# Optimization experiments

Measured on AMD Instinct MI355X. Metric: run time of the kernel, lower is better.

The kernel has to match this reference:

```python
import jax, jax.numpy as jnp
import numpy as np

B, L, D = 4, 1024, 768
H, Dh = 12, 64
W_ONE_SIDED = 512


def setup_inputs() -> dict:
    key = jax.random.key(0)
    ks = jax.random.split(key, 14)
    std = 0.02
    def lin(k):
        return jax.random.normal(k, (D, D), jnp.float32) * std
    inp = {
        "hidden_states": jax.random.normal(ks[0], (B, L, D), jnp.float32),
        "Wq": lin(ks[1]), "bq": jnp.zeros((D,), jnp.float32),
        "Wk": lin(ks[2]), "bk": jnp.zeros((D,), jnp.float32),
        "Wv": lin(ks[3]), "bv": jnp.zeros((D,), jnp.float32),
        "Wqg": lin(ks[4]), "bqg": jnp.zeros((D,), jnp.float32),
        "Wkg": lin(ks[5]), "bkg": jnp.zeros((D,), jnp.float32),
        "Wvg": lin(ks[6]), "bvg": jnp.zeros((D,), jnp.float32),
    }
    pos = jnp.arange(L)
    # last 64 positions padded; first 8 tokens are global (CLS-like)
    inp["is_index_masked"] = jnp.broadcast_to(pos >= L - 64, (B, L))
    inp["is_index_global_attn"] = jnp.broadcast_to(pos < 8, (B, L))
    return inp


def _split_heads(x):
    # [B, L, D] -> [B, L, H, Dh]
    return x.reshape(B, L, H, Dh)


def reference(hidden_states, Wq, bq, Wk, bk, Wv, bv, Wqg, bqg, Wkg, bkg, Wvg, bvg,
              is_index_masked, is_index_global_attn):
    scale = 1.0 / np.sqrt(Dh)
    x = hidden_states
    Ql = _split_heads(x @ Wq + bq)
    Kl = _split_heads(x @ Wk + bk)
    Vl = _split_heads(x @ Wv + bv)
    Qg = _split_heads(x @ Wqg + bqg)
    Kg = _split_heads(x @ Wkg + bkg)
    Vg = _split_heads(x @ Wvg + bvg)

    neg_inf = jnp.finfo(x.dtype).min
    not_masked = ~is_index_masked
    not_global = ~is_index_global_attn

    # ---- local branch: doubled-K scores [B,H,L,2L] (first half: global-key
    # columns, second half: banded local-key columns), joint softmax ----
    s = jnp.einsum('bqhd,bkhd->bhqk', Ql, Kl) * scale  # [B,H,L,L]
    idx = jnp.arange(L)
    band = jnp.abs(idx[None, :] - idx[:, None]) <= W_ONE_SIDED  # [L,L]
    global_valid = (is_index_global_attn & not_masked)[:, None, None, :]      # [B,1,1,L]
    local_valid = (band[None, :, :] & (not_masked & not_global)[:, None, :])[:, None, :, :]  # [B,1,L,L]
    s_first = jnp.where(global_valid, s, neg_inf)
    s_second = jnp.where(local_valid, s, neg_inf)
    scores_local = jnp.concatenate([s_first, s_second], axis=-1)  # [B,H,L,2L]
    probs = jax.nn.softmax(scores_local.astype(jnp.float32), axis=-1).astype(x.dtype)
    probs = jnp.where(is_index_masked[:, None, :, None], 0.0, probs)
    # (p1 + p2) @ V  ==  p1 @ V + p2 @ V  since K/V are duplicated
    p_sum = probs[..., :L] + probs[..., L:]
    attn_local = jnp.einsum('bhqk,bkhd->bqhd', p_sum, Vl).reshape(B, L, D)

    # ---- global branch: full attention over global projections ----
    sg = jnp.einsum('bqhd,bkhd->bhqk', Qg, Kg) * scale
    sg = jnp.where(is_index_masked[:, None, None, :], neg_inf, sg)
    pg = jax.nn.softmax(sg.astype(jnp.float32), axis=-1).astype(x.dtype)
    pg = jnp.where(is_index_masked[:, None, :, None], 0.0, pg)
    attn_global = jnp.einsum('bhqk,bkhd->bqhd', pg, Vg).reshape(B, L, D)

    # ---- gated combine: global tokens take the global-attention output ----
    output = jnp.where(is_index_global_attn[:, :, None], attn_global, attn_local)
    return output
```

## Files before the change

### kernel.cpp

```cpp
#include <hip/hip_runtime.h>
#include <stdint.h>
#include <math.h>

#define LSEQ 1024
#define NB 4
#define DM 768
#define NHEAD 12
#define HD 64
#define LVALID 960
#define WIN 512

typedef unsigned short u16;
typedef __attribute__((ext_vector_type(8))) short s16x8;
typedef __attribute__((ext_vector_type(4))) float f32x4;

__device__ __forceinline__ u16 f2bf(float f) {
  union { float f; uint32_t u; } v; v.f = f;
  uint32_t r = v.u + 0x7fffu + ((v.u >> 16) & 1u);
  return (u16)(r >> 16);
}
__device__ __forceinline__ float bf2f(u16 h) {
  union { uint32_t u; float f; } v; v.u = ((uint32_t)h) << 16;
  return v.f;
}
__device__ __forceinline__ int swz8(int row, int chunk) {
  return row * 8 + (chunk ^ (row & 7));
}

__device__ __forceinline__ void gload_lds16(const void* g, void* l) {
  __builtin_amdgcn_global_load_lds(
      (const __attribute__((address_space(1))) unsigned int*)g,
      (__attribute__((address_space(3))) unsigned int*)l, 16, 0, 0);
}

struct WPtrs { const float* w[6]; };
struct GemmPtrs { const u16* wt[6]; const float* bias[6]; u16* out[6]; };

__global__ __launch_bounds__(256) void prep(const float* __restrict__ x, u16* __restrict__ xb,
                                            WPtrs P, u16* __restrict__ wtb) {
  int bi = blockIdx.x;
  if (bi >= 864) {
    int i = ((bi - 864) * 256 + threadIdx.x) * 8;
    float4 a = *(const float4*)(x + i);
    float4 bq = *(const float4*)(x + i + 4);
    u16 t[8];
    t[0] = f2bf(a.x); t[1] = f2bf(a.y); t[2] = f2bf(a.z); t[3] = f2bf(a.w);
    t[4] = f2bf(bq.x); t[5] = f2bf(bq.y); t[6] = f2bf(bq.z); t[7] = f2bf(bq.w);
    *(uint4*)(xb + i) = *(uint4*)t;
    return;
  }
  int mat = bi / 144, rem = bi - mat * 144;
  int gx = rem % 12, gy = rem / 12;
  const float* W = P.w[mat];
  u16* Wt = wtb + (size_t)mat * DM * DM;
  __shared__ u16 tile[64][72];
  int k0 = gx * 64, n0 = gy * 64;
  int r4 = threadIdx.x >> 4;
  int c4 = (threadIdx.x & 15) * 4;
#pragma unroll
  for (int it = 0; it < 4; it++) {
    int r = it * 16 + r4;
    float4 v = *(const float4*)(W + (size_t)(k0 + r) * DM + n0 + c4);
    tile[c4 + 0][r] = f2bf(v.x);
    tile[c4 + 1][r] = f2bf(v.y);
    tile[c4 + 2][r] = f2bf(v.z);
    tile[c4 + 3][r] = f2bf(v.w);
  }
  __syncthreads();
  int rw = threadIdx.x >> 3, cw = (threadIdx.x & 7) * 8;
#pragma unroll
  for (int it = 0; it < 2; it++) {
    int r = it * 32 + rw;
    *(uint4*)(Wt + (size_t)(n0 + r) * DM + k0 + cw) = *(uint4*)&tile[r][cw];
  }
}

__global__ __launch_bounds__(256) void gemm6(const u16* __restrict__ Xb, GemmPtrs P,
                                             u16* __restrict__ Vt) {
  int mat = blockIdx.z;
  int m0 = blockIdx.x * 128, n0 = blockIdx.y * 128;
  if (mat == 3 && (m0 & 1023) != 0) return;
  __shared__ u16 SMEM[128 * 64 * 2];
  u16* As = SMEM;
  u16* Bs = SMEM + 128 * 64;
  const u16* Wt = P.wt[mat];
  int tid = threadIdx.x;
  int w = tid >> 6, lane = tid & 63, qd = lane >> 4, l16 = lane & 15;
  int wm = w & 1, wn = w >> 1;
  f32x4 acc[4][4];
  const f32x4 fz = {0.f, 0.f, 0.f, 0.f};
#pragma unroll
  for (int i = 0; i < 4; i++)
#pragma unroll
    for (int j = 0; j < 4; j++) acc[i][j] = fz;

  int rowS[4], colS[4];
#pragma unroll
  for (int i = 0; i < 4; i++) {
    int s = (w * 4 + i) * 64 + lane;
    rowS[i] = s >> 3;
    colS[i] = ((s & 7) ^ (rowS[i] & 7)) * 8;
  }

  for (int kt = 0; kt < DM; kt += 64) {
    __syncthreads();
#pragma unroll
    for (int i = 0; i < 4; i++)
      gload_lds16(Xb + (size_t)(m0 + rowS[i]) * DM + kt + colS[i],
                  As + (size_t)(w * 4 + i) * 64 * 8);
#pragma unroll
    for (int i = 0; i < 4; i++)
      gload_lds16(Wt + (size_t)(n0 + rowS[i]) * DM + kt + colS[i],
                  Bs + (size_t)(w * 4 + i) * 64 * 8);
    __syncthreads();
#pragma unroll
    for (int ks = 0; ks < 2; ks++) {
      s16x8 af[4], bf[4];
#pragma unroll
      for (int mi = 0; mi < 4; mi++)
        af[mi] = *(const s16x8*)(As + swz8(wm * 64 + mi * 16 + l16, ks * 4 + qd) * 8);
#pragma unroll
      for (int ni = 0; ni < 4; ni++)
        bf[ni] = *(const s16x8*)(Bs + swz8(wn * 64 + ni * 16 + l16, ks * 4 + qd) * 8);
#pragma unroll
      for (int mi = 0; mi < 4; mi++)
#pragma unroll
        for (int ni = 0; ni < 4; ni++)
          acc[mi][ni] = __builtin_amdgcn_mfma_f32_16x16x32_bf16(af[mi], bf[ni], acc[mi][ni], 0, 0, 0);
    }
  }

  const float* bias = P.bias[mat];
  u16* outp = P.out[mat];
  int bb = m0 >> 10, t0 = m0 & 1023;
  __syncthreads();
  u16* Cs = SMEM;
#pragma unroll
  for (int ni = 0; ni < 4; ni++) {
    int n = wn * 64 + ni * 16 + l16;
    float bvl = bias[n0 + n];
#pragma unroll
    for (int mi = 0; mi < 4; mi++) {
      int mb = wm * 64 + mi * 16 + qd * 4;
      u16 pk[4];
#pragma unroll
      for (int r = 0; r < 4; r++) {
        u16 v = f2bf(acc[mi][ni][r] + bvl);
        Cs[(mb + r) * 128 + n] = v;
        pk[r] = v;
      }
      if (mat == 2) {
        int gn = n0 + n, hh = gn >> 6, dd = gn & 63;
        *(uint2*)(Vt + ((size_t)(bb * NHEAD + hh) * HD + dd) * LSEQ + t0 + mb) =
            *(uint2*)pk;
      }
    }
  }
  __syncthreads();
#pragma unroll
  for (int it = 0; it < 8; it++) {
    int c = it * 256 + tid;
    int row = c >> 4, col = c & 15;
    *(uint4*)(outp + (size_t)(m0 + row) * DM + n0 + col * 8) = ((const uint4*)Cs)[c];
  }
}

__global__ __launch_bounds__(128) void attn_local(
    const u16* __restrict__ Qb, const u16* __restrict__ Kb,
    const u16* __restrict__ Vt, float* __restrict__ out) {
  int q0 = blockIdx.x * 32, h = blockIdx.y, b = blockIdx.z;
  __shared__ u16 Ks[64 * 64], Vs[64 * 64];
  __shared__ u16 Ps[2][16 * 64];
  int tid = threadIdx.x, w = tid >> 6, lane = tid & 63, qd = lane >> 4, l16 = lane & 15;

  int rowK[4], colK[4];
#pragma unroll
  for (int i = 0; i < 4; i++) {
    int s = (w * 4 + i) * 64 + lane;
    rowK[i] = s >> 3;
    colK[i] = ((s & 7) ^ (rowK[i] & 7)) * 8;
  }

  const u16* qrow = Qb + (size_t)(b * LSEQ + q0 + w * 16 + l16) * DM + h * HD;
  s16x8 af0 = *(const s16x8*)(qrow + qd * 8);
  s16x8 af1 = *(const s16x8*)(qrow + 32 + qd * 8);

  float l_part[4] = {0.f, 0.f, 0.f, 0.f};
  f32x4 aO[4];
  const f32x4 fz = {0.f, 0.f, 0.f, 0.f};
#pragma unroll
  for (int nt = 0; nt < 4; nt++) aO[nt] = fz;

  for (int c = 0; c < 16; c++) {
    int kb = c * 64;
    if (c > 0 && !(kb < LVALID && kb + 63 >= q0 - WIN && kb <= q0 + 31 + WIN)) continue;
    __syncthreads();
#pragma unroll
    for (int i = 0; i < 4; i++) {
      gload_lds16(Kb + (size_t)(b * LSEQ + kb + rowK[i]) * DM + h * HD + colK[i],
                  Ks + (size_t)(w * 4 + i) * 512);
      gload_lds16(Vt + (size_t)((b * NHEAD + h) * HD + rowK[i]) * LSEQ + kb + colK[i],
                  Vs + (size_t)(w * 4 + i) * 512);
    }
    __syncthreads();

    float p[4][4];
#pragma unroll
    for (int nt = 0; nt < 4; nt++) {
      s16x8 bk0 = *(const s16x8*)(Ks + swz8(nt * 16 + l16, qd) * 8);
      s16x8 bk1 = *(const s16x8*)(Ks + swz8(nt * 16 + l16, 4 + qd) * 8);
      f32x4 s = fz;
      s = __builtin_amdgcn_mfma_f32_16x16x32_bf16(af0, bk0, s, 0, 0, 0);
      s = __builtin_amdgcn_mfma_f32_16x16x32_bf16(af1, bk1, s, 0, 0, 0);
      int k = kb + nt * 16 + l16;
#pragma unroll
      for (int r = 0; r < 4; r++) {
        int q = q0 + w * 16 + qd * 4 + r;
        bool valid = (k < 8) || (k < LVALID && (k - q) <= WIN && (q - k) <= WIN);
        float sv = valid ? s[r] * 0.125f : -1e30f;
        p[nt][r] = __expf(sv);
        l_part[r] += p[nt][r];
      }
    }

#pragma unroll
    for (int nt = 0; nt < 4; nt++) {
      int chunk = nt * 2 + (l16 >> 3);
      int within = l16 & 7;
#pragma unroll
      for (int r = 0; r < 4; r++) {
        int qrow2 = qd * 4 + r;
        Ps[w][swz8(qrow2, chunk) * 8 + within] = f2bf(p[nt][r]);
      }
    }

    s16x8 pf0 = *(const s16x8*)(&Ps[w][0] + swz8(l16, qd) * 8);
    s16x8 pf1 = *(const s16x8*)(&Ps[w][0] + swz8(l16, 4 + qd) * 8);
#pragma unroll
    for (int nt = 0; nt < 4; nt++) {
      s16x8 v0 = *(const s16x8*)(Vs + swz8(nt * 16 + l16, qd) * 8);
      s16x8 v1 = *(const s16x8*)(Vs + swz8(nt * 16 + l16, 4 + qd) * 8);
      aO[nt] = __builtin_amdgcn_mfma_f32_16x16x32_bf16(pf0, v0, aO[nt], 0, 0, 0);
      aO[nt] = __builtin_amdgcn_mfma_f32_16x16x32_bf16(pf1, v1, aO[nt], 0, 0, 0);
    }
  }

#pragma unroll
  for (int off = 1; off < 16; off <<= 1)
#pragma unroll
    for (int r = 0; r < 4; r++) l_part[r] += __shfl_xor(l_part[r], off);
  float inv[4];
#pragma unroll
  for (int r = 0; r < 4; r++) inv[r] = 1.0f / l_part[r];
#pragma unroll
  for (int nt = 0; nt < 4; nt++)
#pragma unroll
    for (int r = 0; r < 4; r++) {
      int q = q0 + w * 16 + qd * 4 + r;
      out[(size_t)(b * LSEQ + q) * DM + h * HD + nt * 16 + l16] = aO[nt][r] * inv[r];
    }
}

__global__ __launch_bounds__(256) void attn_global(
    const u16* __restrict__ Qgb, const u16* __restrict__ Kgb,
    const u16* __restrict__ Vgb, float* __restrict__ out) {
  int h = blockIdx.x, b = blockIdx.y;
  __shared__ float p_lds[8][960];
  __shared__ float partial[4][8][64];
  int tid = threadIdx.x, w = tid >> 6, lane = tid & 63, qd = lane >> 4, l16 = lane & 15;

  {
    float4 z = {0.f, 0.f, 0.f, 0.f};
#pragma unroll
    for (int it = 0; it < 4; it++) {
      int idx = it * 256 + tid;
      int r = idx >> 4, cc = idx & 15;
      *(float4*)(out + (size_t)(b * LSEQ + LVALID + r) * DM + h * HD + cc * 4) = z;
    }
  }

  const u16* qbase = Qgb + (size_t)(b * LSEQ + l16) * DM + h * HD;
  s16x8 af0 = *(const s16x8*)(qbase + qd * 8);
  s16x8 af1 = *(const s16x8*)(qbase + 32 + qd * 8);
  const f32x4 fz = {0.f, 0.f, 0.f, 0.f};
#pragma unroll
  for (int t = 0; t < 15; t++) {
    int kb = (w + 4 * t) * 16;
    const u16* kbase = Kgb + (size_t)(b * LSEQ + kb + l16) * DM + h * HD;
    s16x8 bk0 = *(const s16x8*)(kbase + qd * 8);
    s16x8 bk1 = *(const s16x8*)(kbase + 32 + qd * 8);
    f32x4 s = fz;
    s = __builtin_amdgcn_mfma_f32_16x16x32_bf16(af0, bk0, s, 0, 0, 0);
    s = __builtin_amdgcn_mfma_f32_16x16x32_bf16(af1, bk1, s, 0, 0, 0);
    if (qd < 2) {
#pragma unroll
      for (int r = 0; r < 4; r++)
        p_lds[qd * 4 + r][kb + l16] = s[r] * 0.125f;
    }
  }
  __syncthreads();

#pragma unroll
  for (int qi = 0; qi < 2; qi++) {
    int q = w * 2 + qi;
    float m = -1e30f;
#pragma unroll
    for (int ki = 0; ki < 15; ki++) m = fmaxf(m, p_lds[q][ki * 64 + lane]);
#pragma unroll
    for (int off = 1; off < 64; off <<= 1) m = fmaxf(m, __shfl_xor(m, off));
    float e[15], ssum = 0.f;
#pragma unroll
    for (int ki = 0; ki < 15; ki++) {
      e[ki] = __expf(p_lds[q][ki * 64 + lane] - m);
      ssum += e[ki];
    }
#pragma unroll
    for (int off = 1; off < 64; off <<= 1) ssum += __shfl_xor(ssum, off);
    float inv = 1.0f / ssum;
#pragma unroll
    for (int ki = 0; ki < 15; ki++) p_lds[q][ki * 64 + lane] = e[ki] * inv;
  }
  __syncthreads();

  float acc[8] = {0.f, 0.f, 0.f, 0.f, 0.f, 0.f, 0.f, 0.f};
  const u16* vcol = Vgb + (size_t)b * LSEQ * DM + h * HD + lane;
  for (int kg = 0; kg < 60; kg++) {
    int k0 = w * 240 + kg * 4;
    float v0 = bf2f(vcol[(size_t)(k0 + 0) * DM]);
    float v1 = bf2f(vcol[(size_t)(k0 + 1) * DM]);
    float v2 = bf2f(vcol[(size_t)(k0 + 2) * DM]);
    float v3 = bf2f(vcol[(size_t)(k0 + 3) * DM]);
#pragma unroll
    for (int q = 0; q < 8; q++) {
      float4 p4 = *(const float4*)&p_lds[q][k0];
      acc[q] += p4.x * v0 + p4.y * v1 + p4.z * v2 + p4.w * v3;
    }
  }
#pragma unroll
  for (int q = 0; q < 8; q++) partial[w][q][lane] = acc[q];
  __syncthreads();
#pragma unroll
  for (int i = 0; i < 2; i++) {
    int idx = tid + 256 * i;
    int q = idx >> 6, d = idx & 63;
    float sum = partial[0][q][d] + partial[1][q][d] + partial[2][q][d] + partial[3][q][d];
    out[(size_t)(b * LSEQ + q) * DM + h * HD + d] = sum;
  }
}

extern "C" void kernel_launch(void* const* d_in, const int* in_sizes, int n_in,
                              void* d_out, int out_size, void* d_ws, size_t ws_size,
                              hipStream_t stream) {
  const float* x = (const float*)d_in[0];
  float* out = (float*)d_out;
  char* ws = (char*)d_ws;

  const size_t XB_SZ = (size_t)4096 * DM * 2;
  const size_t WT_SZ = (size_t)6 * DM * DM * 2;
  const size_t MAT_SZ = (size_t)4096 * DM;
  u16* Xb = (u16*)ws;
  u16* Wt = (u16*)(ws + XB_SZ);
  u16* QKV = (u16*)(ws + XB_SZ + WT_SZ);
  u16* Vt = (u16*)(ws + XB_SZ + WT_SZ + (size_t)6 * MAT_SZ * 2);

  u16* Ql = QKV + 0 * MAT_SZ;
  u16* Kl = QKV + 1 * MAT_SZ;
  u16* Vl = QKV + 2 * MAT_SZ;
  u16* Qg = QKV + 3 * MAT_SZ;
  u16* Kg = QKV + 4 * MAT_SZ;
  u16* Vg = QKV + 5 * MAT_SZ;

  WPtrs wp;
  wp.w[0] = (const float*)d_in[1];
  wp.w[1] = (const float*)d_in[3];
  wp.w[2] = (const float*)d_in[5];
  wp.w[3] = (const float*)d_in[7];
  wp.w[4] = (const float*)d_in[9];
  wp.w[5] = (const float*)d_in[11];
  prep<<<2400, 256, 0, stream>>>(x, Xb, wp, Wt);

  GemmPtrs gp;
  const int bidx[6] = {2, 4, 6, 8, 10, 12};
  u16* outs[6] = {Ql, Kl, Vl, Qg, Kg, Vg};
  for (int i = 0; i < 6; i++) {
    gp.wt[i] = Wt + (size_t)i * DM * DM;
    gp.bias[i] = (const float*)d_in[bidx[i]];
    gp.out[i] = outs[i];
  }
  gemm6<<<dim3(32, 6, 6), 256, 0, stream>>>(Xb, gp, Vt);

  attn_local<<<dim3(30, 12, 4), 128, 0, stream>>>(Ql, Kl, Vt, out);
  attn_global<<<dim3(12, 4), 256, 0, stream>>>(Qg, Kg, Vg, out);
}
```

Baseline: 193.3 us.

## Restructure projection GEMM into 256x256 tiles with double-buffered async LDS prefetch

Rewrites the six-way projection GEMM to use 256x256 output tiles with 512 threads per block. A double-buffered LDS pipeline issues direct global-to-LDS loads for the next k-tile while MFMAs run on the current one. The work is split into four sub-phases with explicit barriers, waitcnt and setprio to interleave loads and matrix math. This cuts the block count to roughly one wave on the device and raises operand reuse per LDS load. In exchange it needs 128KB of LDS per block, limiting occupancy to one block per CU, and depends on fragile hand-placed waits.

```diff
diff --git a/kernel.cpp b/kernel.cpp
--- a/kernel.cpp
+++ b/kernel.cpp
@@ -32,6 +32,16 @@
       (const __attribute__((address_space(1))) unsigned int*)g,
       (__attribute__((address_space(3))) unsigned int*)l, 16, 0, 0);
 }
+
+#define BARW()                                  \
+  do {                                          \
+    asm volatile("" ::: "memory");              \
+    __builtin_amdgcn_s_barrier();               \
+    asm volatile("" ::: "memory");              \
+  } while (0)
+#define LGKM0() asm volatile("s_waitcnt lgkmcnt(0)" ::: "memory")
+#define VMC4() asm volatile("s_waitcnt vmcnt(4)" ::: "memory")
+#define VMC0() asm volatile("s_waitcnt vmcnt(0)" ::: "memory")
 
 struct WPtrs { const float* w[6]; };
 struct GemmPtrs { const u16* wt[6]; const float* bias[6]; u16* out[6]; };
@@ -75,78 +85,165 @@
   }
 }
 
-__global__ __launch_bounds__(256) void gemm6(const u16* __restrict__ Xb, GemmPtrs P,
-                                             u16* __restrict__ Vt) {
+__global__ __launch_bounds__(512, 2) void gemm6(const u16* __restrict__ Xb, GemmPtrs P,
+                                                u16* __restrict__ Vt) {
   int mat = blockIdx.z;
-  int m0 = blockIdx.x * 128, n0 = blockIdx.y * 128;
+  int m0 = blockIdx.x * 256, n0 = blockIdx.y * 256;
   if (mat == 3 && (m0 & 1023) != 0) return;
-  __shared__ u16 SMEM[128 * 64 * 2];
-  u16* As = SMEM;
-  u16* Bs = SMEM + 128 * 64;
+  __shared__ __align__(16) u16 SMEM[65536];
   const u16* Wt = P.wt[mat];
   int tid = threadIdx.x;
   int w = tid >> 6, lane = tid & 63, qd = lane >> 4, l16 = lane & 15;
-  int wm = w & 1, wn = w >> 1;
-  f32x4 acc[4][4];
+  int wm = w >> 2, wn = w & 3;
+  int cx = l16 & 7;
+
+  f32x4 acc[8][4];
   const f32x4 fz = {0.f, 0.f, 0.f, 0.f};
 #pragma unroll
-  for (int i = 0; i < 4; i++)
+  for (int i = 0; i < 8; i++)
 #pragma unroll
     for (int j = 0; j < 4; j++) acc[i][j] = fz;
 
-  int rowS[4], colS[4];
-#pragma unroll
-  for (int i = 0; i < 4; i++) {
-    int s = (w * 4 + i) * 64 + lane;
-    rowS[i] = s >> 3;
-    colS[i] = ((s & 7) ^ (rowS[i] & 7)) * 8;
-  }
-
-  for (int kt = 0; kt < DM; kt += 64) {
-    __syncthreads();
-#pragma unroll
-    for (int i = 0; i < 4; i++)
-      gload_lds16(Xb + (size_t)(m0 + rowS[i]) * DM + kt + colS[i],
-                  As + (size_t)(w * 4 + i) * 64 * 8);
-#pragma unroll
-    for (int i = 0; i < 4; i++)
-      gload_lds16(Wt + (size_t)(n0 + rowS[i]) * DM + kt + colS[i],
-                  Bs + (size_t)(w * 4 + i) * 64 * 8);
-    __syncthreads();
-#pragma unroll
-    for (int ks = 0; ks < 2; ks++) {
-      s16x8 af[4], bf[4];
-#pragma unroll
-      for (int mi = 0; mi < 4; mi++)
-        af[mi] = *(const s16x8*)(As + swz8(wm * 64 + mi * 16 + l16, ks * 4 + qd) * 8);
-#pragma unroll
-      for (int ni = 0; ni < 4; ni++)
-        bf[ni] = *(const s16x8*)(Bs + swz8(wn * 64 + ni * 16 + l16, ks * 4 + qd) * 8);
-#pragma unroll
-      for (int mi = 0; mi < 4; mi++)
-#pragma unroll
-        for (int ni = 0; ni < 4; ni++)
-          acc[mi][ni] = __builtin_amdgcn_mfma_f32_16x16x32_bf16(af[mi], bf[ni], acc[mi][ni], 0, 0, 0);
-    }
-  }
+  int aoff[2][2], boff[2][2];
+#pragma unroll
+  for (int j = 0; j < 2; j++) {
+    int s = j * 512 + tid;
+    int row = s >> 3;
+    int col = ((s & 7) ^ (row & 7)) * 8;
+#pragma unroll
+    for (int h = 0; h < 2; h++) {
+      aoff[j][h] = (m0 + h * 128 + row) * DM + col;
+      boff[j][h] = (n0 + h * 128 + row) * DM + col;
+    }
+  }
+
+  auto stageA = [&](int t, int h) {
+#pragma unroll
+    for (int j = 0; j < 2; j++)
+      gload_lds16(Xb + (size_t)aoff[j][h] + t * 64,
+                  &SMEM[(t & 1) * 32768 + h * 8192 + (j * 512 + w * 64) * 8]);
+  };
+  auto stageB = [&](int t, int h) {
+#pragma unroll
+    for (int j = 0; j < 2; j++)
+      gload_lds16(Wt + (size_t)boff[j][h] + t * 64,
+                  &SMEM[(t & 1) * 32768 + 16384 + h * 8192 + (j * 512 + w * 64) * 8]);
+  };
+
+  stageA(0, 0); stageA(0, 1);
+  stageB(0, 0); stageB(0, 1);
+  stageB(1, 0); stageB(1, 1);
+  VMC4();
+  BARW();
+
+  const int rB = (wn & 1) * 64 + l16;
+
+  auto tile = [&](int u) {
+    const int buf = u & 1;
+    const u16* Ab = &SMEM[buf * 32768 + wm * 8192];
+    const u16* Bb = &SMEM[buf * 32768 + 16384 + (wn >> 1) * 8192];
+    s16x8 af[4][2], bfr[4][2];
+#pragma unroll
+    for (int mi = 0; mi < 4; mi++)
+#pragma unroll
+      for (int ks = 0; ks < 2; ks++)
+        af[mi][ks] = *(const s16x8*)(Ab + (mi * 16 + l16) * 64 + ((ks * 4 + qd) ^ cx) * 8);
+#pragma unroll
+    for (int ni = 0; ni < 2; ni++)
+#pragma unroll
+      for (int ks = 0; ks < 2; ks++)
+        bfr[ni][ks] = *(const s16x8*)(Bb + (rB + ni * 16) * 64 + ((ks * 4 + qd) ^ cx) * 8);
+    if (u < 11) stageA(u + 1, 0);
+    BARW();
+    LGKM0();
+    __builtin_amdgcn_s_setprio(1);
+#pragma unroll
+    for (int mi = 0; mi < 4; mi++)
+#pragma unroll
+      for (int ni = 0; ni < 2; ni++)
+#pragma unroll
+        for (int ks = 0; ks < 2; ks++)
+          acc[mi][ni] = __builtin_amdgcn_mfma_f32_16x16x32_bf16(af[mi][ks], bfr[ni][ks],
+                                                                acc[mi][ni], 0, 0, 0);
+    __builtin_amdgcn_s_setprio(0);
+    BARW();
+#pragma unroll
+    for (int ni = 2; ni < 4; ni++)
+#pragma unroll
+      for (int ks = 0; ks < 2; ks++)
+        bfr[ni][ks] = *(const s16x8*)(Bb + (rB + ni * 16) * 64 + ((ks * 4 + qd) ^ cx) * 8);
+    if (u < 11) stageA(u + 1, 1);
+    BARW();
+    LGKM0();
+    __builtin_amdgcn_s_setprio(1);
+#pragma unroll
+    for (int mi = 0; mi < 4; mi++)
+#pragma unroll
+      for (int ni = 2; ni < 4; ni++)
+#pragma unroll
+        for (int ks = 0; ks < 2; ks++)
+          acc[mi][ni] = __builtin_amdgcn_mfma_f32_16x16x32_bf16(af[mi][ks], bfr[ni][ks],
+                                                                acc[mi][ni], 0, 0, 0);
+    __builtin_amdgcn_s_setprio(0);
+    BARW();
+#pragma unroll
+    for (int mi = 0; mi < 4; mi++)
+#pragma unroll
+      for (int ks = 0; ks < 2; ks++)
+        af[mi][ks] = *(const s16x8*)(Ab + ((mi + 4) * 16 + l16) * 64 + ((ks * 4 + qd) ^ cx) * 8);
+    if (u < 10) stageB(u + 2, 0);
+    BARW();
+    LGKM0();
+    __builtin_amdgcn_s_setprio(1);
+#pragma unroll
+    for (int mi = 0; mi < 4; mi++)
+#pragma unroll
+      for (int ni = 0; ni < 2; ni++)
+#pragma unroll
+        for (int ks = 0; ks < 2; ks++)
+          acc[mi + 4][ni] = __builtin_amdgcn_mfma_f32_16x16x32_bf16(af[mi][ks], bfr[ni][ks],
+                                                                    acc[mi + 4][ni], 0, 0, 0);
+    __builtin_amdgcn_s_setprio(0);
+    BARW();
+    if (u < 10) {
+      stageB(u + 2, 1);
+      VMC4();
+    } else {
+      VMC0();
+    }
+    BARW();
+    __builtin_amdgcn_s_setprio(1);
+#pragma unroll
+    for (int mi = 0; mi < 4; mi++)
+#pragma unroll
+      for (int ni = 2; ni < 4; ni++)
+#pragma unroll
+        for (int ks = 0; ks < 2; ks++)
+          acc[mi + 4][ni] = __builtin_amdgcn_mfma_f32_16x16x32_bf16(af[mi][ks], bfr[ni][ks],
+                                                                    acc[mi + 4][ni], 0, 0, 0);
+    __builtin_amdgcn_s_setprio(0);
+    BARW();
+  };
+
+  for (int u = 0; u < 12; ++u) tile(u);
 
   const float* bias = P.bias[mat];
   u16* outp = P.out[mat];
   int bb = m0 >> 10, t0 = m0 & 1023;
   __syncthreads();
-  u16* Cs = SMEM;
+  u16* Cs = &SMEM[0];
 #pragma unroll
   for (int ni = 0; ni < 4; ni++) {
     int n = wn * 64 + ni * 16 + l16;
     float bvl = bias[n0 + n];
 #pragma unroll
-    for (int mi = 0; mi < 4; mi++) {
-      int mb = wm * 64 + mi * 16 + qd * 4;
+    for (int mi = 0; mi < 8; mi++) {
+      int mb = wm * 128 + mi * 16 + qd * 4;
       u16 pk[4];
 #pragma unroll
       for (int r = 0; r < 4; r++) {
         u16 v = f2bf(acc[mi][ni][r] + bvl);
-        Cs[(mb + r) * 128 + n] = v;
+        Cs[(mb + r) * 256 + n] = v;
         pk[r] = v;
       }
       if (mat == 2) {
@@ -158,9 +255,9 @@
   }
   __syncthreads();
 #pragma unroll
-  for (int it = 0; it < 8; it++) {
-    int c = it * 256 + tid;
-    int row = c >> 4, col = c & 15;
+  for (int it = 0; it < 16; it++) {
+    int c = it * 512 + tid;
+    int row = c >> 5, col = c & 31;
     *(uint4*)(outp + (size_t)(m0 + row) * DM + n0 + col * 8) = ((const uint4*)Cs)[c];
   }
 }
@@ -387,7 +484,7 @@
     gp.bias[i] = (const float*)d_in[bidx[i]];
     gp.out[i] = outs[i];
   }
-  gemm6<<<dim3(32, 6, 6), 256, 0, stream>>>(Xb, gp, Vt);
+  gemm6<<<dim3(16, 3, 6), 512, 0, stream>>>(Xb, gp, Vt);
 
   attn_local<<<dim3(30, 12, 4), 128, 0, stream>>>(Ql, Kl, Vt, out);
   attn_global<<<dim3(12, 4), 256, 0, stream>>>(Qg, Kg, Vg, out);
```

Result: slower. 201.2 us (+4.0%).
